# Optimization experiments

Hardware: AMD Instinct MI355X
Metric: run time of the kernel (lower is better)

## Reference

```python
import jax, jax.numpy as jnp
import numpy as np

B, S, DIM = 4, 1024, 2048
N_HEAD, N_KV, HEAD_DIM = 32, 8, 64


def setup_inputs() -> dict:
    key = jax.random.key(0)
    k1, k2, k3, k4 = jax.random.split(key, 4)
    x = jax.random.normal(k1, (B, S, DIM), dtype=jnp.float32)
    # rotary table: [S, head_dim//2, 2] = (cos, sin)
    inv_freq = 1.0 / (10000.0 ** (jnp.arange(0, HEAD_DIM, 2, dtype=jnp.float32) / HEAD_DIM))
    t = jnp.arange(S, dtype=jnp.float32)
    ang = t[:, None] * inv_freq[None, :]
    freqs_cis = jnp.stack([jnp.cos(ang), jnp.sin(ang)], axis=-1)
    mask = jnp.tril(jnp.ones((S, S), dtype=bool))[None, None]  # causal bool [1,1,S,S]
    scale = 0.02
    wqkv = jax.random.normal(k2, ((N_HEAD + 2 * N_KV) * HEAD_DIM, DIM), dtype=jnp.float32) * scale
    wo = jax.random.normal(k3, (DIM, DIM), dtype=jnp.float32) * scale
    return {"x": x, "freqs_cis": freqs_cis, "mask": mask, "wqkv": wqkv, "wo": wo}


def _apply_rotary(x, freqs_cis):
    # x: [b, s, h, d]; freqs_cis: [s, d//2, 2]
    b, s, h, d = x.shape
    xr = x.reshape(b, s, h, d // 2, 2)
    fc = freqs_cis.reshape(1, s, 1, d // 2, 2)
    cos, sin = fc[..., 0], fc[..., 1]
    x0, x1 = xr[..., 0], xr[..., 1]
    out = jnp.stack([x0 * cos - x1 * sin, x1 * cos + x0 * sin], axis=-1)
    return out.reshape(b, s, h, d)


def reference(x, freqs_cis, mask, wqkv, wo):
    b, s, _ = x.shape
    qkv = jnp.einsum('bsd,ed->bse', x, wqkv)
    q, k, v = jnp.split(qkv, [N_HEAD * HEAD_DIM, (N_HEAD + N_KV) * HEAD_DIM], axis=-1)
    q = q.reshape(b, s, N_HEAD, HEAD_DIM)
    k = k.reshape(b, s, N_KV, HEAD_DIM)
    v = v.reshape(b, s, N_KV, HEAD_DIM)
    q = _apply_rotary(q, freqs_cis)
    k = _apply_rotary(k, freqs_cis)
    # [b, h, s, d]
    q = q.transpose(0, 2, 1, 3)
    k = k.transpose(0, 2, 1, 3)
    v = v.transpose(0, 2, 1, 3)
    g = N_HEAD // N_KV
    k = jnp.repeat(k, g, axis=1)
    v = jnp.repeat(v, g, axis=1)
    scale = 1.0 / np.sqrt(HEAD_DIM).astype(np.float32)
    scores = jnp.einsum('bhqd,bhkd->bhqk', q, k) * scale
    scores = jnp.where(mask, scores, jnp.float32(-jnp.inf))
    attn = jax.nn.softmax(scores, axis=-1)
    y = jnp.einsum('bhqk,bhkd->bhqd', attn, v)
    y = y.transpose(0, 2, 1, 3).reshape(b, s, DIM)
    return jnp.einsum('bsd,ed->bse', y, wo)
```

## Files before the change

### kernel.cpp

```cpp
#include <hip/hip_runtime.h>
#include <stdint.h>

typedef __bf16 bf16;
typedef __attribute__((ext_vector_type(8))) __bf16 bf16x8;
typedef __attribute__((ext_vector_type(4))) __bf16 bf16x4;
typedef __attribute__((ext_vector_type(4))) float f32x4;
typedef __attribute__((ext_vector_type(16))) float f32x16;
typedef __attribute__((ext_vector_type(2))) unsigned u32x2;

#define AS1 __attribute__((address_space(1)))
#define AS3 __attribute__((address_space(3)))

#if __has_builtin(__builtin_amdgcn_permlane32_swap)
#define HAVE_PLSWAP 1
#else
#define HAVE_PLSWAP 0
#endif

__device__ __forceinline__ float ex2(float x) {
#if __has_builtin(__builtin_amdgcn_exp2f)
  return __builtin_amdgcn_exp2f(x);
#else
  return exp2f(x);
#endif
}

__device__ __forceinline__ void barrier_f() {
  asm volatile("" ::: "memory");
  __builtin_amdgcn_s_barrier();
  asm volatile("" ::: "memory");
}

template <int N>
__device__ __forceinline__ void waitVm() {
  if constexpr (N == 0) asm volatile("s_waitcnt vmcnt(0)" ::: "memory");
  else if constexpr (N == 1) asm volatile("s_waitcnt vmcnt(1)" ::: "memory");
  else if constexpr (N == 2) asm volatile("s_waitcnt vmcnt(2)" ::: "memory");
  else if constexpr (N == 4) asm volatile("s_waitcnt vmcnt(4)" ::: "memory");
  else if constexpr (N == 6) asm volatile("s_waitcnt vmcnt(6)" ::: "memory");
  else if constexpr (N == 8) asm volatile("s_waitcnt vmcnt(8)" ::: "memory");
  else static_assert(N == 0, "unsupported vmcnt");
  __builtin_amdgcn_sched_barrier(0);
}

__device__ __forceinline__ u32x2 swap32(uint32_t a, uint32_t b, int hh) {
#if HAVE_PLSWAP
  (void)hh;
  return __builtin_amdgcn_permlane32_swap(a, b, false, false);
#else
  u32x2 r;
  r[0] = hh ? __shfl_xor(b, 32) : a;
  r[1] = hh ? b : __shfl_xor(a, 32);
  return r;
#endif
}

template <int K>
__device__ __forceinline__ void relay_body(const float* __restrict__ W,
                                           bf16* __restrict__ Bp, int t) {
  const int off = t * 8;
  const int sub = (off & 511) >> 3;
  const int n = sub & 15, khi = sub >> 4;
  const int blk = off >> 9;
  const int kblk = blk & ((K >> 5) - 1);
  const int nblk = blk >> (31 - __builtin_clz(K >> 5));
  const float* src = W + (size_t)(nblk * 16 + n) * K + kblk * 32 + khi * 8;
  float4 a = *reinterpret_cast<const float4*>(src);
  float4 b = *reinterpret_cast<const float4*>(src + 4);
  bf16x8 o = { (bf16)a.x, (bf16)a.y, (bf16)a.z, (bf16)a.w,
               (bf16)b.x, (bf16)b.y, (bf16)b.z, (bf16)b.w };
  *reinterpret_cast<bf16x8*>(Bp + off) = o;
}

__global__ __launch_bounds__(256) void prologue_kernel(
    const float* __restrict__ x, bf16* __restrict__ xb,
    const float* __restrict__ wqkv, bf16* __restrict__ BpQ,
    const float* __restrict__ wo, bf16* __restrict__ BpO) {
  const int blk = blockIdx.x;
  if (blk < 8192) {
    const int i = blk * 256 + threadIdx.x;
    float4 v = reinterpret_cast<const float4*>(x)[i];
    bf16x4 r = { (bf16)v.x, (bf16)v.y, (bf16)v.z, (bf16)v.w };
    reinterpret_cast<bf16x4*>(xb)[i] = r;
  } else if (blk < 11264) {
    relay_body<2048>(wqkv, BpQ, (blk - 8192) * 256 + threadIdx.x);
  } else {
    relay_body<2048>(wo, BpO, (blk - 11264) * 256 + threadIdx.x);
  }
}

template <int BN, typename OutT, bool FUSE, int MINW>
__global__ __launch_bounds__(512, MINW) void gemmfc2(
    const bf16* __restrict__ A, const bf16* __restrict__ Bp,
    OutT* __restrict__ C, const float* __restrict__ fc,
    bf16* __restrict__ Qd, bf16* __restrict__ Kd, bf16* __restrict__ Vd,
    int N, int K) {
  constexpr int WTN = BN / 8;
  constexpr int NR = WTN / 16;
  constexpr int NBF = 2 * NR;
  constexpr int ABUF = 64 * 128;
  __shared__ char smem[2 * ABUF];
  AS3 char* sm3 = (AS3 char*)smem;

  const int tid = threadIdx.x;
  const int w = tid >> 6, lane = tid & 63;
  const int fr = lane & 15, fq = lane >> 4;
  const int xorA = (fr & 7) << 4;

  const int orig = blockIdx.x;
  const int cpx = (int)gridDim.x >> 3;
  const int wgid = (orig & 7) * cpx + (orig >> 3);
  const int bm = (wgid & 63) * 64;
  const int bn = (wgid >> 6) * BN;
  const int KB = K >> 5;
  const int nbBase = (bn >> 4) + w * NR;

  f32x4 acc[4][NR] = {};

  auto stageA = [&](int t, int buf) {
    AS3 char* db = sm3 + buf * ABUF;
    const int row = tid >> 3;
    const int kslot = (tid & 7) ^ (row & 7);
    __builtin_amdgcn_global_load_lds(
        (const AS1 void*)(A + (size_t)(bm + row) * K + t * 64 + kslot * 8),
        (AS3 void*)(db + w * 1024), 16, 0, 0);
  };

  stageA(0, 0);

  const int NT = K >> 6;
  for (int t = 0; t < NT; ++t) {
    const int cb = t & 1;
    const bool pf = (t + 1 < NT);
    bf16x8 bF[NR][2];
#pragma unroll
    for (int ni = 0; ni < NR; ++ni)
#pragma unroll
      for (int ks = 0; ks < 2; ++ks)
        bF[ni][ks] = *reinterpret_cast<const bf16x8*>(
            Bp + ((size_t)(nbBase + ni) * KB + t * 2 + ks) * 512 + lane * 8);
    waitVm<NBF>();
    barrier_f();
    if (pf) stageA(t + 1, cb ^ 1);
    const char* cbA = smem + cb * ABUF;
    bf16x8 aF[2][2];
#pragma unroll
    for (int mi = 0; mi < 2; ++mi)
#pragma unroll
      for (int ks = 0; ks < 2; ++ks)
        aF[mi][ks] = *reinterpret_cast<const bf16x8*>(
            cbA + (mi * 16 + fr) * 128 + ((ks * 64 + fq * 16) ^ xorA));
    if (pf) waitVm<1>(); else waitVm<0>();
#pragma unroll
    for (int mp = 0; mp < 2; ++mp) {
      if (mp > 0) {
#pragma unroll
        for (int mi = 0; mi < 2; ++mi)
#pragma unroll
          for (int ks = 0; ks < 2; ++ks)
            aF[mi][ks] = *reinterpret_cast<const bf16x8*>(
                cbA + (32 + mi * 16 + fr) * 128 + ((ks * 64 + fq * 16) ^ xorA));
      }
      __builtin_amdgcn_s_setprio(1);
#pragma unroll
      for (int ks = 0; ks < 2; ++ks)
#pragma unroll
        for (int mi = 0; mi < 2; ++mi)
#pragma unroll
          for (int ni = 0; ni < NR; ++ni)
            acc[mp * 2 + mi][ni] = __builtin_amdgcn_mfma_f32_16x16x32_bf16(
                aF[mi][ks], bF[ni][ks], acc[mp * 2 + mi][ni], 0, 0, 0);
      __builtin_amdgcn_s_setprio(0);
    }
  }

  if constexpr (FUSE) {
    barrier_f();
    float* smF = (float*)smem;
    {
      const float* fsrc = fc + (size_t)(bm & 1023) * 64;
#pragma unroll
      for (int k = 0; k < 2; ++k)
        reinterpret_cast<float4*>(smF)[tid + k * 512] =
            reinterpret_cast<const float4*>(fsrc)[tid + k * 512];
    }
    __syncthreads();
    const float QSCALE = 0.125f * 1.4426950408889634f;
    const int par = fr & 1;
#pragma unroll
    for (int ni = 0; ni < NR; ++ni) {
      const int col = bn + w * WTN + ni * 16 + fr;
#pragma unroll
      for (int mi = 0; mi < 4; ++mi) {
        const int sl = mi * 16 + fq * 4;
        const int row0 = bm + sl;
        const int bb = row0 >> 10, s0 = row0 & 1023;
        if (col < 2560) {
          const int e = (col < 2048) ? col : col - 2048;
          const int d = e & 63, hq = e >> 6;
          const int dbase = d & ~1;
          bf16* dst = (col < 2048)
              ? Qd + (((size_t)(bb * 32 + hq)) * 1024 + s0) * 64 + d
              : Kd + (((size_t)(bb * 8 + hq)) * 1024 + s0) * 64 + d;
#pragma unroll
          for (int j = 0; j < 4; ++j) {
            float v = acc[mi][ni][j];
            float pv = __shfl_xor(v, 1);
            float2 csn = *reinterpret_cast<const float2*>(
                &smF[(sl + j) * 64 + dbase]);
            float r = par ? (v * csn.x + pv * csn.y)
                          : (v * csn.x - pv * csn.y);
            if (col < 2048) r *= QSCALE;
            dst[(size_t)j * 64] = (bf16)r;
          }
        } else {
          const int e = col - 2560, d = e & 63, hv = e >> 6;
          bf16x4 pk4;
#pragma unroll
          for (int j = 0; j < 4; ++j) pk4[j] = (bf16)acc[mi][ni][j];
          *reinterpret_cast<bf16x4*>(
              Vd + (((size_t)(bb * 8 + hv)) * 64 + d) * 1024 + s0) = pk4;
        }
      }
    }
  } else {
    const int cbn = bn + w * WTN + fr;
#pragma unroll
    for (int mi = 0; mi < 4; ++mi) {
      const int rb = bm + mi * 16 + fq * 4;
#pragma unroll
      for (int ni = 0; ni < NR; ++ni)
#pragma unroll
        for (int j = 0; j < 4; ++j)
          C[(size_t)(rb + j) * N + cbn + ni * 16] = (OutT)acc[mi][ni][j];
    }
  }
}

__global__ __launch_bounds__(256, 4) void attn_kernel(const bf16* __restrict__ Q,
                                                      const bf16* __restrict__ K,
                                                      const bf16* __restrict__ Vt,
                                                      bf16* __restrict__ Y) {
  __shared__ bf16 smem[25600];
  char* sb = (char*)smem;
  AS3 char* sA = (AS3 char*)smem;

  const int fid = blockIdx.x;
  const int hkv = fid & 7;
  const int hl = (fid >> 3) & 3;
  const int b = (fid >> 5) & 3;
  const int j = (fid >> 7) & 3;
  const int h = hkv * 4 + hl;

  const int w = threadIdx.x >> 6, lane = threadIdx.x & 63;
  const int qn = lane & 31;
  const int hh = lane >> 5;
  const int srow = lane >> 3;
  const int scb = (((lane & 7) ^ srow) << 4);
  const int xsw = (qn & 7) << 4;

  const bf16* Qh = Q + ((size_t)(b * 32 + h)) * 65536;
  const char* kB = (const char*)(K + ((size_t)(b * 8 + hkv)) * 65536);
  const char* vB = (const char*)(Vt + ((size_t)(b * 8 + hkv)) * 65536);

  const int nchA = 2 * j + 2;
  const int TOT = 18;

  auto stage = [&](int ci, int buf) {
    const int kc = ci << 6;
    const int bo = buf * 8192;
#pragma unroll
    for (int i = 0; i < 2; ++i) {
      const int row = i * 32 + 8 * w + srow;
      __builtin_amdgcn_global_load_lds(
          (const AS1 void*)(kB + (size_t)(kc + row) * 128 + scb),
          (AS3 void*)(sA + bo + i * 4096 + w * 1024), 16, 0, 0);
      __builtin_amdgcn_global_load_lds(
          (const AS1 void*)(vB + (size_t)row * 2048 + kc * 2 + scb),
          (AS3 void*)(sA + 16384 + bo + i * 4096 + w * 1024), 16, 0, 0);
    }
  };

  auto applyMask = [&](f32x16* st, int kc, int qg) {
#pragma unroll
    for (int mt = 0; mt < 2; ++mt)
#pragma unroll
      for (int r = 0; r < 16; ++r) {
        int kv = kc + mt * 32 + (r & 3) + 8 * (r >> 2) + 4 * hh;
        if (kv > qg) st[mt][r] = -3e38f;
      }
  };

  union F32U { float f; uint32_t u; };
  union W64 { uint32_t u; bf16 b[2]; };

  int tq0 = j * 128 + w * 32;
  int maskFrom = tq0 >> 6;
  bf16x8 qf[4];
#pragma unroll
  for (int s = 0; s < 4; ++s)
    qf[s] = *reinterpret_cast<const bf16x8*>(
        &Qh[(size_t)(tq0 + qn) * 64 + s * 16 + hh * 8]);
  f32x16 O[2] = {};
  float mrow = -3e38f, lrow = 0.f;

  auto epilogue = [&]() {
    float inv = 1.f / lrow;
    bf16* Ytw = smem + 16384 + w * 2304;
#pragma unroll
    for (int dt = 0; dt < 2; ++dt)
#pragma unroll
      for (int r = 0; r < 16; ++r) {
        int d = dt * 32 + (r & 3) + 8 * (r >> 2) + 4 * hh;
        Ytw[qn * 72 + d] = (bf16)(O[dt][r] * inv);
      }
    asm volatile("s_waitcnt lgkmcnt(0)" ::: "memory");
    const int qr = lane >> 1, c0 = (lane & 1) * 32;
    bf16* yout = Y + ((size_t)(b * 1024 + tq0 - w * 32 + (w * 32) + qr)) * 2048 + h * 64 + c0;
#pragma unroll
    for (int i = 0; i < 4; ++i)
      *reinterpret_cast<bf16x8*>(&yout[i * 8]) =
          *reinterpret_cast<const bf16x8*>(&Ytw[qr * 72 + c0 + i * 8]);
  };

  stage(0, 0);

  for (int s = 0; s < TOT; ++s) {
    const int cur = s & 1;
    const int c = (s < nchA) ? s : s - nchA;
    if (s + 1 < TOT) {
      stage((s + 1 < nchA) ? s + 1 : s + 1 - nchA, cur ^ 1);
      waitVm<4>();
    } else {
      waitVm<0>();
    }
    barrier_f();
    const int kc = c << 6;
    const char* Kc = sb + cur * 8192;
    const char* Vc = sb + 16384 + cur * 8192;

    bf16x8 kf[2][4];
#pragma unroll
    for (int mt = 0; mt < 2; ++mt)
#pragma unroll
      for (int si = 0; si < 4; ++si)
        kf[mt][si] = *reinterpret_cast<const bf16x8*>(
            Kc + (qn + 32 * mt) * 128 + ((32 * si + 16 * hh) ^ xsw));
    f32x16 st[2] = {};
#pragma unroll
    for (int mt = 0; mt < 2; ++mt)
#pragma unroll
      for (int si = 0; si < 4; ++si)
        st[mt] = __builtin_amdgcn_mfma_f32_32x32x16_bf16(kf[mt][si], qf[si], st[mt], 0, 0, 0);
    if (c >= maskFrom) applyMask(st, kc, tq0 + qn);
    float t16[16];
#pragma unroll
    for (int i = 0; i < 16; ++i) t16[i] = fmaxf(st[0][i], st[1][i]);
#pragma unroll
    for (int off = 8; off >= 1; off >>= 1)
#pragma unroll
      for (int i = 0; i < off; ++i) t16[i] = fmaxf(t16[i], t16[i + off]);
    F32U fm; fm.f = t16[0];
    u32x2 rm = swap32(fm.u, fm.u, hh);
    F32U m0, m1; m0.u = rm[0]; m1.u = rm[1];
    float mx = fmaxf(m0.f, m1.f);
    if (!__all(mx - mrow <= 8.f)) {
      float mnew = fmaxf(mrow, mx);
      float alpha = ex2(mrow - mnew);
      lrow *= alpha;
#pragma unroll
      for (int dt = 0; dt < 2; ++dt)
#pragma unroll
        for (int r = 0; r < 16; ++r) O[dt][r] *= alpha;
      mrow = mnew;
    }
    W64 pk[2][8];
    float ps[16];
#pragma unroll
    for (int t = 0; t < 2; ++t)
#pragma unroll
      for (int wi = 0; wi < 8; ++wi) {
        float p0 = ex2(st[t][2 * wi] - mrow);
        float p1 = ex2(st[t][2 * wi + 1] - mrow);
        ps[t * 8 + wi] = p0 + p1;
        pk[t][wi].b[0] = (bf16)p0;
        pk[t][wi].b[1] = (bf16)p1;
      }
#pragma unroll
    for (int off = 8; off >= 1; off >>= 1)
#pragma unroll
      for (int i = 0; i < off; ++i) ps[i] += ps[i + off];
    F32U fs; fs.f = ps[0];
    u32x2 rs = swap32(fs.u, fs.u, hh);
    F32U s0, s1; s0.u = rs[0]; s1.u = rs[1];
    lrow += s0.f + s1.f;
#pragma unroll
    for (int si = 0; si < 4; ++si) {
      const int t = si >> 1, a0 = 4 * (si & 1);
      u32x2 rA = swap32(pk[t][a0 + 0].u, pk[t][a0 + 2].u, hh);
      u32x2 rB = swap32(pk[t][a0 + 1].u, pk[t][a0 + 3].u, hh);
      union BF { uint32_t u[4]; bf16x8 v; } bfrag;
      bfrag.u[0] = rA[0];
      bfrag.u[1] = rB[0];
      bfrag.u[2] = rA[1];
      bfrag.u[3] = rB[1];
#pragma unroll
      for (int dt = 0; dt < 2; ++dt) {
        bf16x8 vf = *reinterpret_cast<const bf16x8*>(
            Vc + (qn + 32 * dt) * 128 + ((32 * si + 16 * hh) ^ xsw));
        O[dt] = __builtin_amdgcn_mfma_f32_32x32x16_bf16(vf, bfrag.v, O[dt], 0, 0, 0);
      }
    }
    barrier_f();

    if (s == nchA - 1) {
      const int nq0 = (7 - j) * 128 + w * 32;
      bf16x8 nqf[4];
#pragma unroll
      for (int si = 0; si < 4; ++si)
        nqf[si] = *reinterpret_cast<const bf16x8*>(
            &Qh[(size_t)(nq0 + qn) * 64 + si * 16 + hh * 8]);
      epilogue();
      tq0 = nq0;
      maskFrom = tq0 >> 6;
#pragma unroll
      for (int si = 0; si < 4; ++si) qf[si] = nqf[si];
#pragma unroll
      for (int dt = 0; dt < 2; ++dt)
#pragma unroll
        for (int r = 0; r < 16; ++r) O[dt][r] = 0.f;
      mrow = -3e38f;
      lrow = 0.f;
    }
  }

  epilogue();
}

extern "C" void kernel_launch(void* const* d_in, const int* in_sizes, int n_in,
                              void* d_out, int out_size, void* d_ws, size_t ws_size,
                              hipStream_t stream) {
  const float* x    = (const float*)d_in[0];
  const float* fc   = (const float*)d_in[1];
  const float* wqkv = (const float*)d_in[3];
  const float* wo   = (const float*)d_in[4];
  float* out = (float*)d_out;

  char* ws = (char*)d_ws;
  const size_t MB = 1u << 20;
  bf16* xb    = (bf16*)(ws);
  bf16* BpQ   = (bf16*)(ws + 16 * MB);
  bf16* BpO   = (bf16*)(ws + 28 * MB);
  bf16* Qr    = (bf16*)(ws + 60 * MB);
  bf16* Kr    = (bf16*)(ws + 76 * MB);
  bf16* Vt    = (bf16*)(ws + 80 * MB);
  bf16* Y     = (bf16*)(ws + 84 * MB);

  prologue_kernel<<<13312, 256, 0, stream>>>(x, xb, wqkv, BpQ, wo, BpO);

  gemmfc2<384, bf16, true, 4><<<512, 512, 0, stream>>>(
      xb, BpQ, (bf16*)nullptr, fc, Qr, Kr, Vt, 3072, 2048);

  attn_kernel<<<512, 256, 0, stream>>>(Qr, Kr, Vt, Y);

  gemmfc2<512, float, false, 2><<<256, 512, 0, stream>>>(
      Y, BpO, out, nullptr, nullptr, nullptr, nullptr, 2048, 2048);
}
```

Measured before the change: 153.2 us.

## Replace output-projection GEMM with dedicated 32x32 MFMA kernel and smaller tiles

Adds a specialized kernel for the Wo projection that uses 32x32x16 bf16 MFMAs, 64x256 block tiles, and direct global-to-LDS loads for A with XOR swizzling. B fragments are read straight from global memory in the pre-packed layout. The launch goes from 256 to 512 blocks so more blocks run on the GPU's CUs. The cost is lower data reuse per block and B reads that bypass LDS, both of which raise global and L2 traffic.

```diff
diff --git a/kernel.cpp b/kernel.cpp
--- a/kernel.cpp
+++ b/kernel.cpp
@@ -237,6 +237,83 @@
   }
 }
 
+__global__ __launch_bounds__(512, 4) void gemm_wo32(
+    const bf16* __restrict__ A, const bf16* __restrict__ Bp,
+    float* __restrict__ C, int N, int K) {
+  constexpr int ABUF = 64 * 128;
+  __shared__ char smem[2 * ABUF];
+  AS3 char* sm3 = (AS3 char*)smem;
+
+  const int tid = threadIdx.x;
+  const int w = tid >> 6, lane = tid & 63;
+  const int qn = lane & 31, hh = lane >> 5;
+  const int wr = w >> 2, wc = w & 3;
+
+  const int orig = blockIdx.x;
+  const int cpx = (int)gridDim.x >> 3;
+  const int wgid = (orig & 7) * cpx + (orig >> 3);
+  const int bm = (wgid & 63) * 64;
+  const int bn = (wgid >> 6) * 256;
+  const int KB = K >> 5;
+  const int nbB = (bn >> 4) + wc * 4 + ((lane >> 4) & 1);
+
+  f32x16 acc2[2] = {};
+
+  auto stageA = [&](int t, int buf) {
+    AS3 char* db = sm3 + buf * ABUF;
+    const int row = tid >> 3;
+    const int kslot = (tid & 7) ^ (row & 7);
+    __builtin_amdgcn_global_load_lds(
+        (const AS1 void*)(A + (size_t)(bm + row) * K + t * 64 + kslot * 8),
+        (AS3 void*)(db + w * 1024), 16, 0, 0);
+  };
+
+  stageA(0, 0);
+
+  const int xorR = (qn & 7) << 4;
+  const int NT = K >> 6;
+  for (int t = 0; t < NT; ++t) {
+    const int cb = t & 1;
+    const bool pf = (t + 1 < NT);
+    bf16x8 bF2[2][4];
+#pragma unroll
+    for (int nt = 0; nt < 2; ++nt)
+#pragma unroll
+      for (int s = 0; s < 4; ++s)
+        bF2[nt][s] = *reinterpret_cast<const bf16x8*>(
+            Bp + ((size_t)(nbB + nt * 2) * KB + t * 2 + (s >> 1)) * 512 +
+            ((s & 1) * 2 + hh) * 128 + (lane & 15) * 8);
+    waitVm<8>();
+    barrier_f();
+    if (pf) stageA(t + 1, cb ^ 1);
+    const char* cbA = smem + cb * ABUF;
+    bf16x8 aF2[4];
+#pragma unroll
+    for (int s = 0; s < 4; ++s)
+      aF2[s] = *reinterpret_cast<const bf16x8*>(
+          cbA + (wr * 32 + qn) * 128 + (((2 * s + hh) << 4) ^ xorR));
+    if (pf) waitVm<1>(); else waitVm<0>();
+    __builtin_amdgcn_s_setprio(1);
+#pragma unroll
+    for (int s = 0; s < 4; ++s)
+#pragma unroll
+      for (int nt = 0; nt < 2; ++nt)
+        acc2[nt] = __builtin_amdgcn_mfma_f32_32x32x16_bf16(
+            aF2[s], bF2[nt][s], acc2[nt], 0, 0, 0);
+    __builtin_amdgcn_s_setprio(0);
+  }
+
+#pragma unroll
+  for (int nt = 0; nt < 2; ++nt) {
+    const int col = bn + wc * 64 + nt * 32 + qn;
+#pragma unroll
+    for (int r = 0; r < 16; ++r) {
+      const int row = bm + wr * 32 + (r & 3) + 8 * (r >> 2) + 4 * hh;
+      C[(size_t)row * N + col] = acc2[nt][r];
+    }
+  }
+}
+
 __global__ __launch_bounds__(256, 4) void attn_kernel(const bf16* __restrict__ Q,
                                                       const bf16* __restrict__ K,
                                                       const bf16* __restrict__ Vt,
@@ -463,6 +540,5 @@
 
   attn_kernel<<<512, 256, 0, stream>>>(Qr, Kr, Vt, Y);
 
-  gemmfc2<512, float, false, 2><<<256, 512, 0, stream>>>(
-      Y, BpO, out, nullptr, nullptr, nullptr, nullptr, 2048, 2048);
-}
+  gemm_wo32<<<512, 512, 0, stream>>>(Y, BpO, out, 2048, 2048);
+}
```

New measurement: 170.6 us. +11.4%, slower.
